# Optimization experiments

Hardware: AMD Instinct MI355X
Metric: run time of the kernel (lower is better)

## Reference

```python
import jax, jax.numpy as jnp
import numpy as np

L, B, D_IN, D = 96, 32, 4, 128   # leaves, batch, input feats, dim_feedforward
NB, NC = 3, 6                    # n_blocks, n_classes
E = L * (L - 1)                  # directed edges, no self-loops


def _adjacency():
    # one-hot receiver/sender matrices, shape (E, L)
    pairs = np.array([(i, j) for i in range(L) for j in range(L) if i != j])
    recv, send = pairs[:, 0], pairs[:, 1]
    rr = np.zeros((E, L), np.float32); rr[np.arange(E), recv] = 1.0
    rs = np.zeros((E, L), np.float32); rs[np.arange(E), send] = 1.0
    return rr, rs


def setup_inputs() -> dict:
    key = jax.random.key(0)
    ks = jax.random.split(key, 24)
    rr, rs = _adjacency()
    inp = {
        'inputs': jax.random.normal(ks[0], (L, B, D_IN), jnp.float32),
        'rel_rec': jnp.broadcast_to(jnp.asarray(rr), (B, E, L)),
        'rel_send': jnp.broadcast_to(jnp.asarray(rs), (B, E, L)),
    }
    s = 0.1
    # initial MLP: D_IN -> D -> D
    inp['W0a'] = s * jax.random.normal(ks[1], (D_IN, D)); inp['b0a'] = jnp.zeros((D,))
    inp['W0b'] = s * jax.random.normal(ks[2], (D, D));    inp['b0b'] = jnp.zeros((D,))
    # per-block edge MLP (2D -> D -> D) and node MLP (D -> D -> D), stacked over NB
    inp['eW1'] = s * jax.random.normal(ks[3], (NB, 2 * D, D)); inp['eb1'] = jnp.zeros((NB, D))
    inp['eW2'] = s * jax.random.normal(ks[4], (NB, D, D));     inp['eb2'] = jnp.zeros((NB, D))
    inp['nW1'] = s * jax.random.normal(ks[5], (NB, D, D));     inp['nb1'] = jnp.zeros((NB, D))
    inp['nW2'] = s * jax.random.normal(ks[6], (NB, D, D));     inp['nb2'] = jnp.zeros((NB, D))
    # final MLP: 2D -> D -> NC
    inp['fW1'] = s * jax.random.normal(ks[7], (2 * D, D)); inp['fb1'] = jnp.zeros((D,))
    inp['fW2'] = s * jax.random.normal(ks[8], (D, NC));    inp['fb2'] = jnp.zeros((NC,))
    return inp


def _mlp(x, W1, b1, W2, b2):
    return jax.nn.elu(jax.nn.elu(x @ W1 + b1) @ W2 + b2)


def reference(inputs, rel_rec, rel_send, W0a, b0a, W0b, b0b,
              eW1, eb1, eW2, eb2, nW1, nb1, nW2, nb2,
              fW1, fb1, fW2, fb2):
    def node2edge(h):
        # (b,l,d) -> (b,E,2d): cat([senders, receivers])
        senders = jnp.einsum('bel,bld->bed', rel_send, h)
        receivers = jnp.einsum('bel,bld->bed', rel_rec, h)
        return jnp.concatenate([senders, receivers], axis=2)

    def edge2node(h):
        # (b,E,d) -> (b,l,d), mean over incoming edges
        incoming = jnp.einsum('bel,bed->bld', rel_rec, h)
        denom = rel_rec.sum(1)[:, 1]  # (b,)
        return incoming / denom[:, None, None]

    x = jnp.transpose(inputs, (1, 0, 2))           # (b, l, d_in)
    x = _mlp(x, W0a, b0a, W0b, b0b)                # (b, l, D)
    x = node2edge(x)                               # (b, E, 2D)
    for i in range(NB):
        x = _mlp(x, eW1[i], eb1[i], eW2[i], eb2[i])  # (b, E, D)
        x = edge2node(x)                             # (b, l, D)
        x = _mlp(x, nW1[i], nb1[i], nW2[i], nb2[i])  # (b, l, D)
        x = node2edge(x)                             # (b, E, 2D)
    out = jax.nn.elu(x @ fW1 + fb1) @ fW2 + fb2    # (b, E, NC)
    return out
```

## Files before the change

kernel.cpp:

```cpp
#include <hip/hip_runtime.h>
#include <hip/hip_bf16.h>

#define LN 96
#define BN 32
#define DM 128
#define EPN 95

typedef __attribute__((ext_vector_type(8))) short s16x8;
typedef __attribute__((ext_vector_type(4))) float f32x4;

__device__ __forceinline__ float eluf(float x){ return x > 0.f ? x : __expf(x) - 1.f; }
__device__ __forceinline__ unsigned short f2bf(float f){
    unsigned u = __float_as_uint(f);
    return (unsigned short)((u + 0x7fff + ((u >> 16) & 1)) >> 16);
}
__device__ __forceinline__ float bf2f(unsigned short h){ return __uint_as_float(((unsigned)h) << 16); }
__device__ __forceinline__ unsigned cvtpk(float lo, float hi){
    unsigned r;
    asm("v_cvt_pk_bf16_f32 %0, %1, %2" : "=v"(r) : "v"(lo), "v"(hi));
    return r;
}

struct SrcTab { const float* p[19]; };

__global__ void conv_pack_kernel(SrcTab tab, unsigned short* __restrict__ hi,
                                 unsigned short* __restrict__ lo){
    int tid = blockIdx.x * 256 + threadIdx.x;
    int m = tid >> 11, c = tid & 2047;
    int l = c & 63, f = c >> 6;
    int n = (f >> 2) * 16 + (l & 15);
    int k0 = (f & 3) * 32 + (l >> 4) * 8;
    union { unsigned short us[8]; uint4 v; } ph, pl;
#pragma unroll
    for (int e = 0; e < 8; ++e){
        float x;
        if (m == 18) x = (n < 6) ? tab.p[18][(k0 + e) * 6 + n] : 0.f;
        else         x = tab.p[m][(k0 + e) * DM + n];
        unsigned short h = f2bf(x);
        ph.us[e] = h;
        pl.us[e] = f2bf(x - bf2f(h));
    }
    *(uint4*)(hi + (size_t)tid * 8) = ph.v;
    *(uint4*)(lo + (size_t)tid * 8) = pl.v;
}

__device__ __forceinline__ void mmw(const char* atile, int l,
                                    const unsigned short* __restrict__ whW,
                                    const unsigned short* __restrict__ wlW,
                                    f32x4 acc[2]) {
    const int l15 = l & 15, kgrp = l >> 4;
    s16x8 a[4];
#pragma unroll
    for (int ks = 0; ks < 4; ++ks)
        a[ks] = *(const s16x8*)(atile + ((l15 * 256 + (ks * 32 + kgrp * 8) * 2) ^ ((l15 & 7) << 4)));
#pragma unroll
    for (int ntl = 0; ntl < 2; ++ntl) {
#pragma unroll
        for (int ks = 0; ks < 4; ++ks) {
            s16x8 bh = *(const s16x8*)(whW + (size_t)((ntl * 4 + ks) * 64 + l) * 8);
            acc[ntl] = __builtin_amdgcn_mfma_f32_16x16x32_bf16(a[ks], bh, acc[ntl], 0, 0, 0);
        }
#pragma unroll
        for (int ks = 0; ks < 4; ++ks) {
            s16x8 bl = *(const s16x8*)(wlW + (size_t)((ntl * 4 + ks) * 64 + l) * 8);
            acc[ntl] = __builtin_amdgcn_mfma_f32_16x16x32_bf16(a[ks], bl, acc[ntl], 0, 0, 0);
        }
    }
}

__device__ __forceinline__ void store_act(char* atile, int l, int w, f32x4 acc[2]) {
    const int l15 = l & 15, kgrp = l >> 4;
#pragma unroll
    for (int ntl = 0; ntl < 2; ++ntl)
#pragma unroll
        for (int i = 0; i < 4; ++i) {
            int row = kgrp * 4 + i;
            int col = (2 * w + ntl) * 16 + l15;
            *(unsigned short*)(atile + ((row * 256 + col * 2) ^ ((row & 7) << 4))) = f2bf(eluf(acc[ntl][i]));
        }
}

__global__ __launch_bounds__(256) void node0_kernel(
    const float* __restrict__ in,
    const float* __restrict__ W0a, const float* __restrict__ b0a,
    const unsigned short* __restrict__ w2h, const unsigned short* __restrict__ w2l,
    const float* __restrict__ b2,
    const unsigned short* __restrict__ wsh, const unsigned short* __restrict__ wsl,
    const unsigned short* __restrict__ wrh, const unsigned short* __restrict__ wrl,
    const float* __restrict__ bp,
    float* __restrict__ hs, float* __restrict__ hr) {
    __shared__ char atile[16 * 256];
    const int t = threadIdx.x;
    const int q = blockIdx.x >> 5, bblk = blockIdx.x & 31;
    const int row0 = bblk * LN + q * 16;
    const int l = t & 63, w = t >> 6;
    const int l15 = l & 15, kgrp = l >> 4;

    {
        int rr = t >> 4, qq = t & 15, c0 = qq * 8;
        int swz = (rr & 7) << 4;
        union { unsigned short us[8]; uint4 v; } pk;
        int row = row0 + rr;
        int b = row / LN, ll = row - b * LN;
        float4 x = *(const float4*)(in + (size_t)(ll * BN + b) * 4);
#pragma unroll
        for (int j = 0; j < 8; ++j) {
            int cc = c0 + j;
            float a = b0a[cc] + x.x * W0a[cc] + x.y * W0a[DM + cc]
                    + x.z * W0a[2 * DM + cc] + x.w * W0a[3 * DM + cc];
            pk.us[j] = f2bf(eluf(a));
        }
        *(uint4*)(atile + ((rr * 256 + c0 * 2) ^ swz)) = pk.v;
    }
    __syncthreads();

    f32x4 acc[2];
    const int cA = (2 * w) * 16 + l15, cB = (2 * w + 1) * 16 + l15;
    {
        float ba = b2[cA], bb = b2[cB];
        acc[0] = (f32x4){ba, ba, ba, ba};
        acc[1] = (f32x4){bb, bb, bb, bb};
        mmw(atile, l, w2h + w * 4096, w2l + w * 4096, acc);
        __syncthreads();
        store_act(atile, l, w, acc);
        __syncthreads();
    }
    acc[0] = (f32x4){0.f, 0.f, 0.f, 0.f};
    acc[1] = (f32x4){0.f, 0.f, 0.f, 0.f};
    mmw(atile, l, wsh + w * 4096, wsl + w * 4096, acc);
#pragma unroll
    for (int ntl = 0; ntl < 2; ++ntl)
#pragma unroll
        for (int i = 0; i < 4; ++i)
            hs[(size_t)(row0 + kgrp * 4 + i) * DM + (2 * w + ntl) * 16 + l15] = acc[ntl][i];
    {
        float ba = bp[cA], bb = bp[cB];
        acc[0] = (f32x4){ba, ba, ba, ba};
        acc[1] = (f32x4){bb, bb, bb, bb};
        mmw(atile, l, wrh + w * 4096, wrl + w * 4096, acc);
    }
#pragma unroll
    for (int ntl = 0; ntl < 2; ++ntl)
#pragma unroll
        for (int i = 0; i < 4; ++i)
            hr[(size_t)(row0 + kgrp * 4 + i) * DM + (2 * w + ntl) * 16 + l15] = acc[ntl][i];
}

__global__ __launch_bounds__(256) void edge_node_kernel(
    const float* __restrict__ hsIn, const float* __restrict__ hrIn,
    const unsigned short* __restrict__ whi, const unsigned short* __restrict__ wlo,
    int eslot, const float* __restrict__ eb2v,
    int s1, int s2, int sS,
    const float* __restrict__ b1, const float* __restrict__ b2, const float* __restrict__ bp,
    float* __restrict__ hsOut, float* __restrict__ hrOut) {
    __shared__ char tileA[LN * 256];
    __shared__ char tileB[LN * 256];
    __shared__ float hrL[6 * DM];
    __shared__ float gL[6 * DM];
    __shared__ char actA[16 * 256];
    __shared__ char actB[16 * 256];
    const int blk = blockIdx.x;
    const int rg = blk >> 5, b = blk & 31;
    const int r0 = rg * 6;
    const int t = threadIdx.x;
    const int w = t >> 6, l = t & 63;
    const int l15 = l & 15, kgrp = l >> 4;

    if (t < 192) {
        int rr = t >> 5, c4 = (t & 31) * 4;
        *(float4*)(hrL + rr * DM + c4) = *(const float4*)(hrIn + ((size_t)(b * LN + r0 + rr)) * DM + c4);
    }
    s16x8 bfr[2][4];
#pragma unroll
    for (int ntl = 0; ntl < 2; ++ntl)
#pragma unroll
        for (int ks = 0; ks < 4; ++ks)
            bfr[ntl][ks] = *(const s16x8*)(whi + (size_t)eslot * 16384 +
                           (size_t)(((2 * w + ntl) * 4 + ks) * 64 + l) * 8);
    float b20 = eb2v[(2 * w) * 16 + l15], b21 = eb2v[(2 * w + 1) * 16 + l15];
    __syncthreads();

    const float* hsBase = hsIn + (size_t)(b * LN) * DM;
    for (int pr = 0; pr < 3; ++pr) {
        const int rA = r0 + pr * 2, rB = rA + 1;
#pragma unroll
        for (int ch = 0; ch < 6; ++ch) {
            float4 h0[2], h1[2];
            int rrs[2], c0s[2], tts[2];
#pragma unroll
            for (int k = 0; k < 2; ++k) {
                int task = t + (ch * 2 + k) * 256;
                int tt = task >= 1536;
                int rem = task - tt * 1536;
                int rr = rem >> 4, c0 = (rem & 15) * 8;
                rrs[k] = rr; c0s[k] = c0; tts[k] = tt;
                int r = tt ? rB : rA;
                int j = rr + (rr >= r);
                const float* hp = hsBase + (size_t)j * DM + c0;
                h0[k] = *(const float4*)hp;
                h1[k] = *(const float4*)(hp + 4);
            }
#pragma unroll
            for (int k = 0; k < 2; ++k) {
                int rr = rrs[k], c0 = c0s[k], tt = tts[k];
                const float* rp = hrL + (pr * 2 + tt) * DM + c0;
                f32x4 v0 = *(const f32x4*)rp, v1 = *(const f32x4*)(rp + 4);
                float e0 = eluf(h0[k].x + v0[0]), e1 = eluf(h0[k].y + v0[1]);
                float e2 = eluf(h0[k].z + v0[2]), e3 = eluf(h0[k].w + v0[3]);
                float e4 = eluf(h1[k].x + v1[0]), e5 = eluf(h1[k].y + v1[1]);
                float e6 = eluf(h1[k].z + v1[2]), e7 = eluf(h1[k].w + v1[3]);
                uint4 pk;
                pk.x = cvtpk(e0, e1); pk.y = cvtpk(e2, e3);
                pk.z = cvtpk(e4, e5); pk.w = cvtpk(e6, e7);
                *(uint4*)((tt ? tileB : tileA) + ((rr * 256 + c0 * 2) ^ ((rr & 7) << 4))) = pk;
            }
        }
        __syncthreads();
#pragma unroll
        for (int slot = 0; slot < 2; ++slot) {
            const char* tile = slot ? tileB : tileA;
            f32x4 acc[6][2] = {};
#pragma unroll
            for (int mt = 0; mt < 6; ++mt) {
                int arow = mt * 16 + l15;
                const char* rb = tile + arow * 256;
                int swz = (arow & 7) << 4;
#pragma unroll
                for (int ks = 0; ks < 4; ++ks) {
                    s16x8 a = *(const s16x8*)(rb + (((ks * 32 + kgrp * 8) * 2) ^ swz));
                    acc[mt][0] = __builtin_amdgcn_mfma_f32_16x16x32_bf16(a, bfr[0][ks], acc[mt][0], 0, 0, 0);
                    acc[mt][1] = __builtin_amdgcn_mfma_f32_16x16x32_bf16(a, bfr[1][ks], acc[mt][1], 0, 0, 0);
                }
            }
            float cs0 = 0.f, cs1 = 0.f;
#pragma unroll
            for (int mt = 0; mt < 6; ++mt)
#pragma unroll
                for (int i = 0; i < 4; ++i) {
                    int row = mt * 16 + kgrp * 4 + i;
                    if (row < EPN) {
                        cs0 += eluf(acc[mt][0][i] + b20);
                        cs1 += eluf(acc[mt][1][i] + b21);
                    }
                }
            cs0 += __shfl_xor(cs0, 16); cs0 += __shfl_xor(cs0, 32);
            cs1 += __shfl_xor(cs1, 16); cs1 += __shfl_xor(cs1, 32);
            if (l < 16) {
                gL[(pr * 2 + slot) * DM + (2 * w) * 16 + l]     = cs0 * (1.f / 95.f);
                gL[(pr * 2 + slot) * DM + (2 * w + 1) * 16 + l] = cs1 * (1.f / 95.f);
            }
        }
        __syncthreads();
    }

    {
        int rr = t >> 4, q = t & 15, c0 = q * 8;
        int swz = (rr & 7) << 4;
        union { unsigned short us[8]; uint4 v; } pk;
        if (rr < 6) {
            const float* src = gL + rr * DM + c0;
            float4 f0 = *(const float4*)(src);
            float4 f1 = *(const float4*)(src + 4);
            pk.us[0] = f2bf(f0.x); pk.us[1] = f2bf(f0.y); pk.us[2] = f2bf(f0.z); pk.us[3] = f2bf(f0.w);
            pk.us[4] = f2bf(f1.x); pk.us[5] = f2bf(f1.y); pk.us[6] = f2bf(f1.z); pk.us[7] = f2bf(f1.w);
        } else pk.v = make_uint4(0, 0, 0, 0);
        *(uint4*)(actA + ((rr * 256 + c0 * 2) ^ swz)) = pk.v;
    }
    __syncthreads();

    f32x4 acc[2];
    const int cA = (2 * w) * 16 + l15, cB = (2 * w + 1) * 16 + l15;
    {
        float ba = b1[cA], bb = b1[cB];
        acc[0] = (f32x4){ba, ba, ba, ba};
        acc[1] = (f32x4){bb, bb, bb, bb};
        mmw(actA, l, whi + (size_t)s1 * 16384 + w * 4096, wlo + (size_t)s1 * 16384 + w * 4096, acc);
        __syncthreads();
        store_act(actB, l, w, acc);
        __syncthreads();
    }
    {
        float ba = b2[cA], bb = b2[cB];
        acc[0] = (f32x4){ba, ba, ba, ba};
        acc[1] = (f32x4){bb, bb, bb, bb};
        mmw(actB, l, whi + (size_t)s2 * 16384 + w * 4096, wlo + (size_t)s2 * 16384 + w * 4096, acc);
        __syncthreads();
        store_act(actA, l, w, acc);
        __syncthreads();
    }
    acc[0] = (f32x4){0.f, 0.f, 0.f, 0.f};
    acc[1] = (f32x4){0.f, 0.f, 0.f, 0.f};
    mmw(actA, l, whi + (size_t)sS * 16384 + w * 4096, wlo + (size_t)sS * 16384 + w * 4096, acc);
#pragma unroll
    for (int ntl = 0; ntl < 2; ++ntl)
#pragma unroll
        for (int i = 0; i < 4; ++i) {
            int row = kgrp * 4 + i;
            if (row < 6)
                hsOut[(size_t)(b * LN + r0 + row) * DM + (2 * w + ntl) * 16 + l15] = acc[ntl][i];
        }
    {
        float ba = bp[cA], bb = bp[cB];
        acc[0] = (f32x4){ba, ba, ba, ba};
        acc[1] = (f32x4){bb, bb, bb, bb};
        mmw(actA, l, whi + (size_t)(sS + 1) * 16384 + w * 4096, wlo + (size_t)(sS + 1) * 16384 + w * 4096, acc);
    }
#pragma unroll
    for (int ntl = 0; ntl < 2; ++ntl)
#pragma unroll
        for (int i = 0; i < 4; ++i) {
            int row = kgrp * 4 + i;
            if (row < 6)
                hrOut[(size_t)(b * LN + r0 + row) * DM + (2 * w + ntl) * 16 + l15] = acc[ntl][i];
        }
}

__global__ __launch_bounds__(256) void final_kernel(
    const float* __restrict__ hs, const float* __restrict__ hr,
    const unsigned short* __restrict__ wfh, const unsigned short* __restrict__ wfl,
    const float* __restrict__ fb2, float* __restrict__ out) {
    __shared__ char tA[LN * 256];
    __shared__ char tB[LN * 256];
    __shared__ float hrL[6 * DM];
    const int blk = blockIdx.x;
    const int rg = blk >> 5, b = blk & 31;
    const int r0 = rg * 6;
    const int t = threadIdx.x;
    const int w = t >> 6, l = t & 63;
    const int l15 = l & 15, kgrp = l >> 4;

    if (t < 192) {
        int rr = t >> 5, c4 = (t & 31) * 4;
        *(float4*)(hrL + rr * DM + c4) = *(const float4*)(hr + ((size_t)(b * LN + r0 + rr)) * DM + c4);
    }
    s16x8 fh[4], fl4[4];
#pragma unroll
    for (int ks = 0; ks < 4; ++ks) {
        fh[ks]  = *(const s16x8*)(wfh + (size_t)(ks * 64 + l) * 8);
        fl4[ks] = *(const s16x8*)(wfl + (size_t)(ks * 64 + l) * 8);
    }
    float fbv = (l15 < 6) ? fb2[l15] : 0.f;
    __syncthreads();

    const float* hsBase = hs + (size_t)(b * LN) * DM;
    for (int pr = 0; pr < 3; ++pr) {
        const int rA = r0 + pr * 2, rB = rA + 1;
#pragma unroll
        for (int ch = 0; ch < 6; ++ch) {
            float4 h0[2], h1[2];
            int rrs[2], c0s[2], tts[2];
#pragma unroll
            for (int k = 0; k < 2; ++k) {
                int task = t + (ch * 2 + k) * 256;
                int tt = task >= 1536;
                int rem = task - tt * 1536;
                int rr = rem >> 4, c0 = (rem & 15) * 8;
                rrs[k] = rr; c0s[k] = c0; tts[k] = tt;
                int r = tt ? rB : rA;
                int j = rr + (rr >= r);
                const float* hp = hsBase + (size_t)j * DM + c0;
                h0[k] = *(const float4*)hp;
                h1[k] = *(const float4*)(hp + 4);
            }
#pragma unroll
            for (int k = 0; k < 2; ++k) {
                int rr = rrs[k], c0 = c0s[k], tt = tts[k];
                const float* rp = hrL + (pr * 2 + tt) * DM + c0;
                f32x4 v0 = *(const f32x4*)rp, v1 = *(const f32x4*)(rp + 4);
                float e0 = eluf(h0[k].x + v0[0]), e1 = eluf(h0[k].y + v0[1]);
                float e2 = eluf(h0[k].z + v0[2]), e3 = eluf(h0[k].w + v0[3]);
                float e4 = eluf(h1[k].x + v1[0]), e5 = eluf(h1[k].y + v1[1]);
                float e6 = eluf(h1[k].z + v1[2]), e7 = eluf(h1[k].w + v1[3]);
                uint4 pk;
                pk.x = cvtpk(e0, e1); pk.y = cvtpk(e2, e3);
                pk.z = cvtpk(e4, e5); pk.w = cvtpk(e6, e7);
                *(uint4*)((tt ? tB : tA) + ((rr * 256 + c0 * 2) ^ ((rr & 7) << 4))) = pk;
            }
        }
        __syncthreads();
        for (int q = w; q < 12; q += 4) {
            int tt = q >= 6;
            int mt = q - tt * 6;
            const char* tile = tt ? tB : tA;
            int r = tt ? rB : rA;
            int arow = mt * 16 + l15;
            const char* rb = tile + arow * 256;
            int swz = (arow & 7) << 4;
            s16x8 a[4];
#pragma unroll
            for (int ks = 0; ks < 4; ++ks)
                a[ks] = *(const s16x8*)(rb + (((ks * 32 + kgrp * 8) * 2) ^ swz));
            f32x4 acc = (f32x4){fbv, fbv, fbv, fbv};
#pragma unroll
            for (int ks = 0; ks < 4; ++ks)
                acc = __builtin_amdgcn_mfma_f32_16x16x32_bf16(a[ks], fh[ks], acc, 0, 0, 0);
#pragma unroll
            for (int ks = 0; ks < 4; ++ks)
                acc = __builtin_amdgcn_mfma_f32_16x16x32_bf16(a[ks], fl4[ks], acc, 0, 0, 0);
            if (l15 < 6) {
                float* ob = out + ((size_t)b * (LN * EPN) + (size_t)r * EPN) * 6;
#pragma unroll
                for (int i = 0; i < 4; ++i) {
                    int row = mt * 16 + kgrp * 4 + i;
                    if (row < EPN) ob[(size_t)row * 6 + l15] = acc[i];
                }
            }
        }
        __syncthreads();
    }
}

extern "C" void kernel_launch(void* const* d_in, const int* in_sizes, int n_in,
                              void* d_out, int out_size, void* d_ws, size_t ws_size,
                              hipStream_t stream) {
    const float* inputs = (const float*)d_in[0];
    const float* W0a = (const float*)d_in[3];
    const float* b0a = (const float*)d_in[4];
    const float* W0b = (const float*)d_in[5];
    const float* b0b = (const float*)d_in[6];
    const float* eW1 = (const float*)d_in[7];
    const float* eb1 = (const float*)d_in[8];
    const float* eW2 = (const float*)d_in[9];
    const float* eb2 = (const float*)d_in[10];
    const float* nW1 = (const float*)d_in[11];
    const float* nb1 = (const float*)d_in[12];
    const float* nW2 = (const float*)d_in[13];
    const float* nb2 = (const float*)d_in[14];
    const float* fW1 = (const float*)d_in[15];
    const float* fb1 = (const float*)d_in[16];
    const float* fW2 = (const float*)d_in[17];
    const float* fb2 = (const float*)d_in[18];
    float* out = (float*)d_out;

    const int NR = BN * LN;
    unsigned short* whi = (unsigned short*)d_ws;
    unsigned short* wlo = whi + 19 * 16384;
    float* hsA = (float*)(wlo + 19 * 16384);
    float* hrA = hsA + (NR + 1) * DM;
    float* hsB = hrA + NR * DM;
    float* hrB = hsB + (NR + 1) * DM;

    SrcTab tab;
    tab.p[0] = eW2;          tab.p[1] = eW2 + 16384;  tab.p[2] = eW2 + 32768;
    tab.p[3] = W0b;
    tab.p[4] = eW1;          tab.p[5] = eW1 + 16384;
    tab.p[6] = nW1;          tab.p[7] = nW2;          tab.p[8] = eW1 + 32768;  tab.p[9]  = eW1 + 49152;
    tab.p[10] = nW1 + 16384; tab.p[11] = nW2 + 16384; tab.p[12] = eW1 + 65536; tab.p[13] = eW1 + 81920;
    tab.p[14] = nW1 + 32768; tab.p[15] = nW2 + 32768; tab.p[16] = fW1;         tab.p[17] = fW1 + 16384;
    tab.p[18] = fW2;

    #define WM(m) (whi + (m) * 16384), (wlo + (m) * 16384)

    conv_pack_kernel<<<152, 256, 0, stream>>>(tab, whi, wlo);
    node0_kernel<<<192, 256, 0, stream>>>(inputs, W0a, b0a, WM(3), b0b, WM(4), WM(5), eb1, hsA, hrA);
    edge_node_kernel<<<512, 256, 0, stream>>>(hsA, hrA, whi, wlo, 0, eb2,
                                              6, 7, 8, nb1, nb2, eb1 + DM, hsB, hrB);
    edge_node_kernel<<<512, 256, 0, stream>>>(hsB, hrB, whi, wlo, 1, eb2 + DM,
                                              10, 11, 12, nb1 + DM, nb2 + DM, eb1 + 2 * DM, hsA, hrA);
    edge_node_kernel<<<512, 256, 0, stream>>>(hsA, hrA, whi, wlo, 2, eb2 + 2 * DM,
                                              14, 15, 16, nb1 + 2 * DM, nb2 + 2 * DM, fb1, hsB, hrB);
    final_kernel<<<512, 256, 0, stream>>>(hsB, hrB, WM(18), fb2, out);
    #undef WM
}
```

Before: 117.1 us.

## Split edge second-layer GEMM across waves by M-tile with LDS reduction

In the edge MLP's second layer, each wave now takes whole 16-row M-tiles across all 8 N-tiles, instead of every wave walking all M-tiles for its own 2 N-tiles. Each A fragment is therefore read from LDS once instead of by all four waves. Per-wave column sums are combined through a new shared reduction buffer before the mean is written. In exchange, each thread holds the full weight fragment set in registers (8x4 vectors), and the launch bounds now ask for 2 blocks per SIMD, so register pressure and spilling are a risk.

```diff
diff --git a/kernel.cpp b/kernel.cpp
--- a/kernel.cpp
+++ b/kernel.cpp
@@ -146,7 +146,7 @@
             hr[(size_t)(row0 + kgrp * 4 + i) * DM + (2 * w + ntl) * 16 + l15] = acc[ntl][i];
 }
 
-__global__ __launch_bounds__(256) void edge_node_kernel(
+__global__ __launch_bounds__(256, 2) void edge_node_kernel(
     const float* __restrict__ hsIn, const float* __restrict__ hrIn,
     const unsigned short* __restrict__ whi, const unsigned short* __restrict__ wlo,
     int eslot, const float* __restrict__ eb2v,
@@ -159,6 +159,7 @@
     __shared__ float gL[6 * DM];
     __shared__ char actA[16 * 256];
     __shared__ char actB[16 * 256];
+    __shared__ float redbuf[4][2][DM];
     const int blk = blockIdx.x;
     const int rg = blk >> 5, b = blk & 31;
     const int r0 = rg * 6;
@@ -170,14 +171,16 @@
         int rr = t >> 5, c4 = (t & 31) * 4;
         *(float4*)(hrL + rr * DM + c4) = *(const float4*)(hrIn + ((size_t)(b * LN + r0 + rr)) * DM + c4);
     }
-    s16x8 bfr[2][4];
-#pragma unroll
-    for (int ntl = 0; ntl < 2; ++ntl)
+    s16x8 bfr[8][4];
+#pragma unroll
+    for (int nt = 0; nt < 8; ++nt)
 #pragma unroll
         for (int ks = 0; ks < 4; ++ks)
-            bfr[ntl][ks] = *(const s16x8*)(whi + (size_t)eslot * 16384 +
-                           (size_t)(((2 * w + ntl) * 4 + ks) * 64 + l) * 8);
-    float b20 = eb2v[(2 * w) * 16 + l15], b21 = eb2v[(2 * w + 1) * 16 + l15];
+            bfr[nt][ks] = *(const s16x8*)(whi + (size_t)eslot * 16384 +
+                           (size_t)((nt * 4 + ks) * 64 + l) * 8);
+    float b2v[8];
+#pragma unroll
+    for (int nt = 0; nt < 8; ++nt) b2v[nt] = eb2v[nt * 16 + l15];
     __syncthreads();
 
     const float* hsBase = hsIn + (size_t)(b * LN) * DM;
@@ -216,42 +219,64 @@
             }
         }
         __syncthreads();
-#pragma unroll
-        for (int slot = 0; slot < 2; ++slot) {
+        float csum0[8], csum1[8];
+#pragma unroll
+        for (int nt = 0; nt < 8; ++nt) { csum0[nt] = 0.f; csum1[nt] = 0.f; }
+#pragma unroll
+        for (int it = 0; it < 3; ++it) {
+            int qq = w + it * 4;
+            int slot = qq >= 6;
+            int mt = qq - slot * 6;
             const char* tile = slot ? tileB : tileA;
-            f32x4 acc[6][2] = {};
-#pragma unroll
-            for (int mt = 0; mt < 6; ++mt) {
-                int arow = mt * 16 + l15;
-                const char* rb = tile + arow * 256;
-                int swz = (arow & 7) << 4;
-#pragma unroll
-                for (int ks = 0; ks < 4; ++ks) {
-                    s16x8 a = *(const s16x8*)(rb + (((ks * 32 + kgrp * 8) * 2) ^ swz));
-                    acc[mt][0] = __builtin_amdgcn_mfma_f32_16x16x32_bf16(a, bfr[0][ks], acc[mt][0], 0, 0, 0);
-                    acc[mt][1] = __builtin_amdgcn_mfma_f32_16x16x32_bf16(a, bfr[1][ks], acc[mt][1], 0, 0, 0);
-                }
-            }
-            float cs0 = 0.f, cs1 = 0.f;
-#pragma unroll
-            for (int mt = 0; mt < 6; ++mt)
+            int arow = mt * 16 + l15;
+            const char* rb = tile + arow * 256;
+            int swz = (arow & 7) << 4;
+            s16x8 a[4];
+#pragma unroll
+            for (int ks = 0; ks < 4; ++ks)
+                a[ks] = *(const s16x8*)(rb + (((ks * 32 + kgrp * 8) * 2) ^ swz));
+            f32x4 acc[8] = {};
+#pragma unroll
+            for (int nt = 0; nt < 8; ++nt)
+#pragma unroll
+                for (int ks = 0; ks < 4; ++ks)
+                    acc[nt] = __builtin_amdgcn_mfma_f32_16x16x32_bf16(a[ks], bfr[nt][ks], acc[nt], 0, 0, 0);
+            float cs[8];
+#pragma unroll
+            for (int nt = 0; nt < 8; ++nt) {
+                float c = 0.f;
 #pragma unroll
                 for (int i = 0; i < 4; ++i) {
                     int row = mt * 16 + kgrp * 4 + i;
-                    if (row < EPN) {
-                        cs0 += eluf(acc[mt][0][i] + b20);
-                        cs1 += eluf(acc[mt][1][i] + b21);
-                    }
+                    if (row < EPN) c += eluf(acc[nt][i] + b2v[nt]);
                 }
-            cs0 += __shfl_xor(cs0, 16); cs0 += __shfl_xor(cs0, 32);
-            cs1 += __shfl_xor(cs1, 16); cs1 += __shfl_xor(cs1, 32);
-            if (l < 16) {
-                gL[(pr * 2 + slot) * DM + (2 * w) * 16 + l]     = cs0 * (1.f / 95.f);
-                gL[(pr * 2 + slot) * DM + (2 * w + 1) * 16 + l] = cs1 * (1.f / 95.f);
-            }
-        }
-        __syncthreads();
-    }
+                c += __shfl_xor(c, 16); c += __shfl_xor(c, 32);
+                cs[nt] = c;
+            }
+            if (slot == 0) {
+#pragma unroll
+                for (int nt = 0; nt < 8; ++nt) csum0[nt] += cs[nt];
+            } else {
+#pragma unroll
+                for (int nt = 0; nt < 8; ++nt) csum1[nt] += cs[nt];
+            }
+        }
+        if (l < 16) {
+#pragma unroll
+            for (int nt = 0; nt < 8; ++nt) {
+                redbuf[w][0][nt * 16 + l] = csum0[nt];
+                redbuf[w][1][nt * 16 + l] = csum1[nt];
+            }
+        }
+        __syncthreads();
+        if (t < 256) {
+            int slot = t >> 7, col = t & 127;
+            float s = redbuf[0][slot][col] + redbuf[1][slot][col]
+                    + redbuf[2][slot][col] + redbuf[3][slot][col];
+            gL[(pr * 2 + slot) * DM + col] = s * (1.f / 95.f);
+        }
+    }
+    __syncthreads();
 
     {
         int rr = t >> 4, q = t & 15, c0 = q * 8;
```

Result: slower. 131.9 us (+12.6%).
